# Optimization experiments

Measured on AMD Instinct MI355X. Metric: run time of the kernel, lower is better.

Reference implementation:

```python
import jax, jax.numpy as jnp
import numpy as np

B, S, D = 4, 1024, 1024
H, DH = 16, 64
F = 4 * D
EPS = 1e-6


def _ln(x, scale, bias, axes=-1):
    mean = jnp.mean(x, axis=axes, keepdims=True)
    var = jnp.var(x, axis=axes, keepdims=True)
    return (x - mean) * jax.lax.rsqrt(var + EPS) * scale + bias


def setup_inputs() -> dict:
    key = jax.random.key(0)
    ks = jax.random.split(key, 20)
    sd = 1.0 / np.sqrt(D)
    sf = 1.0 / np.sqrt(F)
    inp = {
        'x': jax.random.normal(ks[0], (B, S, D), jnp.float32),
        'z': jax.random.normal(ks[1], (B, S, D), jnp.float32),
        'ln1_s': jnp.ones((D,), jnp.float32),
        'ln1_b': jnp.zeros((D,), jnp.float32),
        'Wq': jax.random.normal(ks[2], (D, D), jnp.float32) * sd,
        'bq': jnp.zeros((D,), jnp.float32),
        'Wk': jax.random.normal(ks[3], (D, D), jnp.float32) * sd,
        'bk': jnp.zeros((D,), jnp.float32),
        'Wv': jax.random.normal(ks[4], (D, D), jnp.float32) * sd,
        'bv': jnp.zeros((D,), jnp.float32),
        'qn_s': jnp.ones((H, DH), jnp.float32),
        'qn_b': jnp.zeros((H, DH), jnp.float32),
        'kn_s': jnp.ones((H, DH), jnp.float32),
        'kn_b': jnp.zeros((H, DH), jnp.float32),
        'Wo': jax.random.normal(ks[5], (D, D), jnp.float32) * sd,
        'bo': jnp.zeros((D,), jnp.float32),
        'ln2_s': jnp.ones((D,), jnp.float32),
        'ln2_b': jnp.zeros((D,), jnp.float32),
        'W1': jax.random.normal(ks[6], (D, F), jnp.float32) * sd,
        'b1': jnp.zeros((F,), jnp.float32),
        'W2': jax.random.normal(ks[7], (D, F), jnp.float32) * sd,
        'b2': jnp.zeros((F,), jnp.float32),
        'W3': jax.random.normal(ks[8], (F, D), jnp.float32) * sf,
        'b3': jnp.zeros((D,), jnp.float32),
    }
    return inp


def reference(x, z, ln1_s, ln1_b, Wq, bq, Wk, bk, Wv, bv, qn_s, qn_b, kn_s, kn_b,
              Wo, bo, ln2_s, ln2_b, W1, b1, W2, b2, W3, b3):
    # z is unused by the original module body
    x_skip = x
    xn = _ln(x, ln1_s, ln1_b)
    q = (xn @ Wq + bq).reshape(B, S, H, DH)
    k = (xn @ Wk + bk).reshape(B, S, H, DH)
    v = (xn @ Wv + bv).reshape(B, S, H, DH)
    # QK-norm: flax LayerNorm(feature_axes=(-2,-1)) still reduces over axis -1,
    # but carries (H, DH)-shaped scale/bias
    q = _ln(q, qn_s, qn_b)
    k = _ln(k, kn_s, kn_b)
    attn = jnp.einsum('bqhd,bkhd->bhqk', q, k) / jnp.sqrt(jnp.asarray(DH, q.dtype))
    attn = jax.nn.softmax(attn, axis=-1)
    out = jnp.einsum('bhqk,bkhd->bqhd', attn, v).reshape(B, S, D)
    x = x_skip + out @ Wo + bo
    x_skip = x
    xn = _ln(x, ln2_s, ln2_b)
    x1 = xn @ W1 + b1
    x2 = xn @ W2 + b2
    h = x1 * jax.nn.gelu(x2, approximate=True)  # GeGLU
    x = x_skip + h @ W3 + b3
    return x
```

## Files before the change

kernel.cpp:

```cpp
#include <hip/hip_runtime.h>

typedef unsigned short u16;
typedef __bf16  bfrag  __attribute__((ext_vector_type(8)));
typedef float   f32x4  __attribute__((ext_vector_type(4)));
typedef u16     u16x8  __attribute__((ext_vector_type(8)));
typedef u16     u16x4  __attribute__((ext_vector_type(4)));

__device__ __forceinline__ float bf2f(u16 u) {
    unsigned v = ((unsigned)u) << 16;
    return __builtin_bit_cast(float, v);
}
__device__ __forceinline__ u16 f2bf(float f) {
    unsigned x = __builtin_bit_cast(unsigned, f);
    unsigned r = (x + 0x7fffu + ((x >> 16) & 1u)) >> 16;
    return (u16)r;
}
__device__ __forceinline__ void g2l16(const u16* g, u16* l) {
    __builtin_amdgcn_global_load_lds((__attribute__((address_space(1))) void*)g,
                                     (__attribute__((address_space(3))) void*)l, 16, 0, 0);
}
__device__ __forceinline__ float gelu_tanh(float x) {
    float c = 1.5957691216057308f * (x + 0.044715f * x * x * x);
    return x * __frcp_rn(1.0f + __expf(-c));
}

#define SWZ(lane)  ((((lane) & 3) ^ (((lane) >> 3) & 3)) * 8)
#define RSWZ(quad, l15)  ((((quad) ^ (((l15) >> 1) & 3))) * 8)

__global__ __launch_bounds__(256) void wt_all(
        const float* __restrict__ Wq, const float* __restrict__ Wk,
        const float* __restrict__ Wv, const float* __restrict__ Wo,
        const float* __restrict__ W1, const float* __restrict__ W2,
        const float* __restrict__ W3,
        u16* __restrict__ WqkvT, u16* __restrict__ WoT,
        u16* __restrict__ W12T, u16* __restrict__ W3T) {
    int blk = blockIdx.x;
    const float* W; u16* Wt; int R, C, local;
    if (blk < 3072) {
        int w = blk >> 10; local = blk & 1023;
        W = (w == 0) ? Wq : (w == 1) ? Wk : Wv;
        Wt = WqkvT + (size_t)w * 1024 * 1024; R = 1024; C = 1024;
    } else if (blk < 4096) { W = Wo; Wt = WoT; R = 1024; C = 1024; local = blk - 3072; }
    else if (blk < 8192)   { W = W1; Wt = W12T; R = 1024; C = 4096; local = blk - 4096; }
    else if (blk < 12288)  { W = W2; Wt = W12T + (size_t)4096 * 1024; R = 1024; C = 4096; local = blk - 8192; }
    else                   { W = W3; Wt = W3T; R = 4096; C = 1024; local = blk - 12288; }
    int tiles_x = C >> 5;
    int c0 = (local % tiles_x) * 32, r0 = (local / tiles_x) * 32;

    __shared__ float tile[32][33];
    int tx = threadIdx.x & 31, ty = threadIdx.x >> 5;
#pragma unroll
    for (int i = 0; i < 32; i += 8)
        tile[ty + i][tx] = W[(size_t)(r0 + ty + i) * C + c0 + tx];
    __syncthreads();
#pragma unroll
    for (int i = 0; i < 32; i += 8)
        Wt[(size_t)(c0 + ty + i) * R + r0 + tx] = f2bf(tile[tx][ty + i]);
}

__global__ __launch_bounds__(256) void ln1024(const float* __restrict__ x,
                                              const float* __restrict__ s,
                                              const float* __restrict__ bi,
                                              u16* __restrict__ out) {
    int row = blockIdx.x, t = threadIdx.x;
    const float4* xr = (const float4*)(x + (size_t)row * 1024);
    float4 v = xr[t];
    float sum = v.x + v.y + v.z + v.w;
    float sq  = v.x * v.x + v.y * v.y + v.z * v.z + v.w * v.w;
#pragma unroll
    for (int off = 1; off < 64; off <<= 1) {
        sum += __shfl_xor(sum, off);
        sq  += __shfl_xor(sq,  off);
    }
    __shared__ float s1[4], s2[4];
    int wave = t >> 6;
    if ((t & 63) == 0) { s1[wave] = sum; s2[wave] = sq; }
    __syncthreads();
    sum = s1[0] + s1[1] + s1[2] + s1[3];
    sq  = s2[0] + s2[1] + s2[2] + s2[3];
    float mean = sum * (1.0f / 1024.0f);
    float var  = sq  * (1.0f / 1024.0f) - mean * mean;
    float inv  = rsqrtf(var + 1e-6f);
    float4 sc = ((const float4*)s)[t], bb = ((const float4*)bi)[t];
    u16x4 o;
    o[0] = f2bf((v.x - mean) * inv * sc.x + bb.x);
    o[1] = f2bf((v.y - mean) * inv * sc.y + bb.y);
    o[2] = f2bf((v.z - mean) * inv * sc.z + bb.z);
    o[3] = f2bf((v.w - mean) * inv * sc.w + bb.w);
    *(u16x4*)&out[(size_t)row * 1024 + t * 4] = o;
}

#define BM 128
#define BK 32
template <int EPI, int BN_, int BSEL>
__global__ __launch_bounds__(256) void gemm_bt(const u16* __restrict__ A,
                                               const u16* __restrict__ Bt,
                                               const float* __restrict__ bias,
                                               const float* __restrict__ bias2,
                                               const float* __restrict__ bias3,
                                               const float* __restrict__ res,
                                               const float* __restrict__ qn_s,
                                               const float* __restrict__ qn_b,
                                               const float* __restrict__ kn_s,
                                               const float* __restrict__ kn_b,
                                               void* __restrict__ Cout,
                                               int M, int N, int K) {
    __shared__ u16 As[BM * BK];
    __shared__ u16 Bs[BN_ * BK];
    constexpr int MI = (BN_ == 128) ? 4 : 2;
    constexpr int NI = 4;
    int tid = threadIdx.x, wave = tid >> 6, lane = tid & 63;
    int quad = lane >> 4, l15 = lane & 15;
    int row0 = blockIdx.y * BM, col0 = blockIdx.x * BN_;
    int wr = (BN_ == 128) ? (wave >> 1) * 64 : wave * 32;
    int wc = (BN_ == 128) ? (wave & 1) * 64 : 0;
    int swz = SWZ(lane);
    int rswz = RSWZ(quad, l15);

    f32x4 acc[MI][NI] = {};

    const u16* gA = A + (size_t)(row0 + wave * 32 + (lane >> 2)) * K + swz;
    u16* lA = &As[wave * 32 * BK];
    const u16* gB;
    u16* lB;
    if (BN_ == 128) { gB = Bt + (size_t)(col0 + wave * 32 + (lane >> 2)) * K + swz; lB = &Bs[wave * 32 * BK]; }
    else            { gB = Bt + (size_t)(col0 + wave * 16 + (lane >> 2)) * K + swz; lB = &Bs[wave * 16 * BK]; }

    for (int k0 = 0; k0 < K; k0 += BK) {
        __syncthreads();
        g2l16(gA + k0,          lA);
        g2l16(gA + k0 + 16 * K, lA + 16 * BK);
        if (BN_ == 128) {
            g2l16(gB + k0,          lB);
            g2l16(gB + k0 + 16 * K, lB + 16 * BK);
        } else {
            g2l16(gB + k0, lB);
        }
        __syncthreads();
        bfrag af[MI], bf[NI];
#pragma unroll
        for (int mi = 0; mi < MI; mi++)
            af[mi] = *(const bfrag*)&As[(wr + mi * 16 + l15) * BK + rswz];
#pragma unroll
        for (int ni = 0; ni < NI; ni++)
            bf[ni] = *(const bfrag*)&Bs[(wc + ni * 16 + l15) * BK + rswz];
#pragma unroll
        for (int mi = 0; mi < MI; mi++)
#pragma unroll
            for (int ni = 0; ni < NI; ni++)
                acc[mi][ni] = __builtin_amdgcn_mfma_f32_16x16x32_bf16(
                    af[mi], bf[ni], acc[mi][ni], 0, 0, 0);
    }

    float bv[NI];
    int cols[NI];
#pragma unroll
    for (int ni = 0; ni < NI; ni++) {
        cols[ni] = col0 + wc + ni * 16 + l15;
        if (BSEL == 1) {
            int seg = cols[ni] >> 10;
            const float* bp = (seg == 0) ? bias : (seg == 1) ? bias2 : bias3;
            bv[ni] = bp[cols[ni] & 1023];
        } else {
            bv[ni] = bias[cols[ni]];
        }
    }

    if (EPI == 4) {
        int cbase = col0 + wc;
        int z = cbase >> 10;
        int hd = (cbase >> 6) & 15;
        float post = (z == 0) ? 0.125f : 1.0f;
        float sn[NI], bn[NI];
        if (z < 2) {
            const float* ns = (z == 0) ? qn_s : kn_s;
            const float* nb = (z == 0) ? qn_b : kn_b;
#pragma unroll
            for (int ni = 0; ni < NI; ni++) {
                sn[ni] = ns[hd * 64 + ni * 16 + l15];
                bn[ni] = nb[hd * 64 + ni * 16 + l15];
            }
        }
#pragma unroll
        for (int mi = 0; mi < MI; mi++) {
            int rbase = row0 + wr + mi * 16 + quad * 4;
#pragma unroll
            for (int r = 0; r < 4; r++) {
                float v0 = acc[mi][0][r] + bv[0];
                float v1 = acc[mi][1][r] + bv[1];
                float v2 = acc[mi][2][r] + bv[2];
                float v3 = acc[mi][3][r] + bv[3];
                size_t rb = (size_t)(rbase + r) * N + cbase;
                if (z == 2) {
                    ((u16*)Cout)[rb + 0 * 16 + l15] = f2bf(v0);
                    ((u16*)Cout)[rb + 1 * 16 + l15] = f2bf(v1);
                    ((u16*)Cout)[rb + 2 * 16 + l15] = f2bf(v2);
                    ((u16*)Cout)[rb + 3 * 16 + l15] = f2bf(v3);
                } else {
                    float s  = v0 + v1 + v2 + v3;
                    float sq = v0 * v0 + v1 * v1 + v2 * v2 + v3 * v3;
#pragma unroll
                    for (int m = 1; m < 16; m <<= 1) {
                        s  += __shfl_xor(s,  m);
                        sq += __shfl_xor(sq, m);
                    }
                    float mean = s * (1.0f / 64.0f);
                    float var  = sq * (1.0f / 64.0f) - mean * mean;
                    float inv  = rsqrtf(var + 1e-6f);
                    ((u16*)Cout)[rb + 0 * 16 + l15] = f2bf(((v0 - mean) * inv * sn[0] + bn[0]) * post);
                    ((u16*)Cout)[rb + 1 * 16 + l15] = f2bf(((v1 - mean) * inv * sn[1] + bn[1]) * post);
                    ((u16*)Cout)[rb + 2 * 16 + l15] = f2bf(((v2 - mean) * inv * sn[2] + bn[2]) * post);
                    ((u16*)Cout)[rb + 3 * 16 + l15] = f2bf(((v3 - mean) * inv * sn[3] + bn[3]) * post);
                }
            }
        }
        return;
    }

#pragma unroll
    for (int mi = 0; mi < MI; mi++) {
        int rbase = row0 + wr + mi * 16 + quad * 4;
#pragma unroll
        for (int r = 0; r < 4; r++) {
            int row = rbase + r;
#pragma unroll
            for (int ni = 0; ni < NI; ni++) {
                float val = acc[mi][ni][r] + bv[ni];
                size_t idx = (size_t)row * N + cols[ni];
                if (EPI == 1) {
                    ((u16*)Cout)[idx] = f2bf(val);
                } else {
                    ((float*)Cout)[idx] = val + res[idx];
                }
            }
        }
    }
}

__global__ __launch_bounds__(256, 2) void gemm_w12(const u16* __restrict__ A,
                                                   const u16* __restrict__ W12T,
                                                   const float* __restrict__ b1,
                                                   const float* __restrict__ b2,
                                                   u16* __restrict__ H) {
    __shared__ u16 As[128 * BK];
    __shared__ u16 B1s[128 * BK];
    __shared__ u16 B2s[128 * BK];
    int tid = threadIdx.x, wave = tid >> 6, lane = tid & 63;
    int quad = lane >> 4, l15 = lane & 15;
    int row0 = blockIdx.y * 128, col0 = blockIdx.x * 128;
    int wr = (wave >> 1) * 64, wc = (wave & 1) * 64;
    int swz = SWZ(lane);
    int rswz = RSWZ(quad, l15);

    f32x4 acc1[4][4] = {}, acc2[4][4] = {};

    const u16* gA  = A    + (size_t)(row0 + wave * 32 + (lane >> 2)) * 1024 + swz;
    const u16* gB1 = W12T + (size_t)(col0 + wave * 32 + (lane >> 2)) * 1024 + swz;
    const u16* gB2 = gB1  + (size_t)4096 * 1024;
    u16* lA  = &As [wave * 32 * BK];
    u16* lB1 = &B1s[wave * 32 * BK];
    u16* lB2 = &B2s[wave * 32 * BK];

    for (int k0 = 0; k0 < 1024; k0 += BK) {
        __syncthreads();
        g2l16(gA  + k0,             lA);
        g2l16(gA  + k0 + 16 * 1024, lA  + 16 * BK);
        g2l16(gB1 + k0,             lB1);
        g2l16(gB1 + k0 + 16 * 1024, lB1 + 16 * BK);
        g2l16(gB2 + k0,             lB2);
        g2l16(gB2 + k0 + 16 * 1024, lB2 + 16 * BK);
        __syncthreads();
        bfrag af[4], b1f[4], b2f[4];
#pragma unroll
        for (int mi = 0; mi < 4; mi++)
            af[mi] = *(const bfrag*)&As[(wr + mi * 16 + l15) * BK + rswz];
#pragma unroll
        for (int ni = 0; ni < 4; ni++) {
            b1f[ni] = *(const bfrag*)&B1s[(wc + ni * 16 + l15) * BK + rswz];
            b2f[ni] = *(const bfrag*)&B2s[(wc + ni * 16 + l15) * BK + rswz];
        }
#pragma unroll
        for (int mi = 0; mi < 4; mi++)
#pragma unroll
            for (int ni = 0; ni < 4; ni++) {
                acc1[mi][ni] = __builtin_amdgcn_mfma_f32_16x16x32_bf16(
                    af[mi], b1f[ni], acc1[mi][ni], 0, 0, 0);
                acc2[mi][ni] = __builtin_amdgcn_mfma_f32_16x16x32_bf16(
                    af[mi], b2f[ni], acc2[mi][ni], 0, 0, 0);
            }
    }

    float bv1[4], bv2[4];
    int cols[4];
#pragma unroll
    for (int ni = 0; ni < 4; ni++) {
        cols[ni] = col0 + wc + ni * 16 + l15;
        bv1[ni] = b1[cols[ni]];
        bv2[ni] = b2[cols[ni]];
    }
#pragma unroll
    for (int mi = 0; mi < 4; mi++) {
        int rbase = row0 + wr + mi * 16 + quad * 4;
#pragma unroll
        for (int r = 0; r < 4; r++) {
#pragma unroll
            for (int ni = 0; ni < 4; ni++) {
                float x1 = acc1[mi][ni][r] + bv1[ni];
                float x2 = acc2[mi][ni][r] + bv2[ni];
                H[(size_t)(rbase + r) * 4096 + cols[ni]] = f2bf(x1 * gelu_tanh(x2));
            }
        }
    }
}

__global__ __launch_bounds__(256) void gemm_splitk(const u16* __restrict__ A,
                                                   const u16* __restrict__ Bt,
                                                   u16* __restrict__ p0,
                                                   u16* __restrict__ p1,
                                                   u16* __restrict__ p2,
                                                   u16* __restrict__ p3) {
    const int K = 4096, N = 1024;
    __shared__ u16 As[128 * BK];
    __shared__ u16 Bs[128 * BK];
    int tid = threadIdx.x, wave = tid >> 6, lane = tid & 63;
    int quad = lane >> 4, l15 = lane & 15;
    int row0 = blockIdx.y * 128, col0 = blockIdx.x * 128;
    int kz = blockIdx.z;
    u16* P = (kz == 0) ? p0 : (kz == 1) ? p1 : (kz == 2) ? p2 : p3;
    int wr = (wave >> 1) * 64, wc = (wave & 1) * 64;
    int swz = SWZ(lane);
    int rswz = RSWZ(quad, l15);

    f32x4 acc[4][4] = {};

    const u16* gA = A  + (size_t)(row0 + wave * 32 + (lane >> 2)) * K + kz * 1024 + swz;
    const u16* gB = Bt + (size_t)(col0 + wave * 32 + (lane >> 2)) * K + kz * 1024 + swz;
    u16* lA = &As[wave * 32 * BK];
    u16* lB = &Bs[wave * 32 * BK];

    for (int k0 = 0; k0 < 1024; k0 += BK) {
        __syncthreads();
        g2l16(gA + k0,          lA);
        g2l16(gA + k0 + 16 * K, lA + 16 * BK);
        g2l16(gB + k0,          lB);
        g2l16(gB + k0 + 16 * K, lB + 16 * BK);
        __syncthreads();
        bfrag af[4], bf[4];
#pragma unroll
        for (int mi = 0; mi < 4; mi++)
            af[mi] = *(const bfrag*)&As[(wr + mi * 16 + l15) * BK + rswz];
#pragma unroll
        for (int ni = 0; ni < 4; ni++)
            bf[ni] = *(const bfrag*)&Bs[(wc + ni * 16 + l15) * BK + rswz];
#pragma unroll
        for (int mi = 0; mi < 4; mi++)
#pragma unroll
            for (int ni = 0; ni < 4; ni++)
                acc[mi][ni] = __builtin_amdgcn_mfma_f32_16x16x32_bf16(
                    af[mi], bf[ni], acc[mi][ni], 0, 0, 0);
    }

#pragma unroll
    for (int mi = 0; mi < 4; mi++) {
        int rbase = row0 + wr + mi * 16 + quad * 4;
#pragma unroll
        for (int r = 0; r < 4; r++)
#pragma unroll
            for (int ni = 0; ni < 4; ni++)
                P[(size_t)(rbase + r) * N + wc + col0 + ni * 16 + l15] =
                    f2bf(acc[mi][ni][r]);
    }
}

__global__ __launch_bounds__(256) void reduce4(const u16* __restrict__ p0,
                                               const u16* __restrict__ p1,
                                               const u16* __restrict__ p2,
                                               const u16* __restrict__ p3,
                                               const float* __restrict__ xmid,
                                               const float* __restrict__ b3,
                                               float* __restrict__ out) {
    size_t i = ((size_t)blockIdx.x * 256 + threadIdx.x) * 4;
    float4 xm = *(const float4*)&xmid[i];
    float4 bb = *(const float4*)&b3[i & 1023];
    u16x4 a0 = *(const u16x4*)&p0[i];
    u16x4 a1 = *(const u16x4*)&p1[i];
    u16x4 a2 = *(const u16x4*)&p2[i];
    u16x4 a3 = *(const u16x4*)&p3[i];
    float4 o;
    o.x = xm.x + bb.x + bf2f(a0[0]) + bf2f(a1[0]) + bf2f(a2[0]) + bf2f(a3[0]);
    o.y = xm.y + bb.y + bf2f(a0[1]) + bf2f(a1[1]) + bf2f(a2[1]) + bf2f(a3[1]);
    o.z = xm.z + bb.z + bf2f(a0[2]) + bf2f(a1[2]) + bf2f(a2[2]) + bf2f(a3[2]);
    o.w = xm.w + bb.w + bf2f(a0[3]) + bf2f(a1[3]) + bf2f(a2[3]) + bf2f(a3[3]);
    *(float4*)&out[i] = o;
}

#define LP 72
__global__ __launch_bounds__(256) void flash(const u16* __restrict__ qkv,
                                             u16* __restrict__ o) {
    int qt = blockIdx.x, h = blockIdx.y, b = blockIdx.z;
    int tid = threadIdx.x, wave = tid >> 6, lane = tid & 63;
    int quad = lane >> 4, l15 = lane & 15;

    __shared__ u16 Qs[128 * LP];
    __shared__ u16 Ks[64 * LP];
    __shared__ u16 Vt[64 * LP];
    __shared__ u16 Ps[128 * LP];

    {
        int row = tid >> 1, half = tid & 1;
        const u16* src = qkv + (size_t)(b * 1024 + qt * 128 + row) * 3072 + h * 64 + half * 32;
        u16* dst = &Qs[row * LP + half * 32];
#pragma unroll
        for (int i = 0; i < 4; i++)
            ((u16x8*)dst)[i] = ((const u16x8*)src)[i];
    }

    f32x4 accO[2][4] = {};
    float m_run[2][4], l_run[2][4];
#pragma unroll
    for (int rt = 0; rt < 2; rt++)
#pragma unroll
        for (int r = 0; r < 4; r++) { m_run[rt][r] = -1e30f; l_run[rt][r] = 0.0f; }

    for (int kt = 0; kt < 16; kt++) {
        __syncthreads();
        {
            int row = tid >> 2, seg = tid & 3;
            size_t gb = (size_t)(b * 1024 + kt * 64 + row) * 3072 + h * 64;
            const u16* ksrc = qkv + gb + 1024 + seg * 16;
            *(u16x8*)&Ks[row * LP + seg * 16]     = *(const u16x8*)ksrc;
            *(u16x8*)&Ks[row * LP + seg * 16 + 8] = *(const u16x8*)(ksrc + 8);
            const u16* vsrc = qkv + gb + 2048 + seg * 16;
            u16x8 v0 = *(const u16x8*)vsrc, v1 = *(const u16x8*)(vsrc + 8);
#pragma unroll
            for (int j = 0; j < 8; j++) Vt[(seg * 16 + j) * LP + row]     = v0[j];
#pragma unroll
            for (int j = 0; j < 8; j++) Vt[(seg * 16 + 8 + j) * LP + row] = v1[j];
        }
        __syncthreads();

        f32x4 accS[2][4] = {};
#pragma unroll
        for (int kk = 0; kk < 2; kk++) {
            bfrag aq[2];
#pragma unroll
            for (int rt = 0; rt < 2; rt++)
                aq[rt] = *(const bfrag*)&Qs[(wave * 32 + rt * 16 + l15) * LP + kk * 32 + quad * 8];
#pragma unroll
            for (int ct = 0; ct < 4; ct++) {
                bfrag bk = *(const bfrag*)&Ks[(ct * 16 + l15) * LP + kk * 32 + quad * 8];
                accS[0][ct] = __builtin_amdgcn_mfma_f32_16x16x32_bf16(aq[0], bk, accS[0][ct], 0, 0, 0);
                accS[1][ct] = __builtin_amdgcn_mfma_f32_16x16x32_bf16(aq[1], bk, accS[1][ct], 0, 0, 0);
            }
        }

#pragma unroll
        for (int rt = 0; rt < 2; rt++) {
#pragma unroll
            for (int r = 0; r < 4; r++) {
                float tmax = accS[rt][0][r];
#pragma unroll
                for (int ct = 1; ct < 4; ct++) tmax = fmaxf(tmax, accS[rt][ct][r]);
#pragma unroll
                for (int m = 1; m < 16; m <<= 1) tmax = fmaxf(tmax, __shfl_xor(tmax, m));
                float mnew  = fmaxf(m_run[rt][r], tmax);
                float alpha = __expf(m_run[rt][r] - mnew);
                float lsum = 0.0f;
                float p[4];
#pragma unroll
                for (int ct = 0; ct < 4; ct++) {
                    p[ct] = __expf(accS[rt][ct][r] - mnew);
                    lsum += p[ct];
                }
#pragma unroll
                for (int m = 1; m < 16; m <<= 1) lsum += __shfl_xor(lsum, m);
                l_run[rt][r] = l_run[rt][r] * alpha + lsum;
                m_run[rt][r] = mnew;
#pragma unroll
                for (int oc = 0; oc < 4; oc++) accO[rt][oc][r] *= alpha;
                int prow = wave * 32 + rt * 16 + quad * 4 + r;
#pragma unroll
                for (int ct = 0; ct < 4; ct++)
                    Ps[prow * LP + ct * 16 + l15] = f2bf(p[ct]);
            }
        }

#pragma unroll
        for (int kk = 0; kk < 2; kk++) {
            bfrag ap[2];
#pragma unroll
            for (int rt = 0; rt < 2; rt++)
                ap[rt] = *(const bfrag*)&Ps[(wave * 32 + rt * 16 + l15) * LP + kk * 32 + quad * 8];
#pragma unroll
            for (int oc = 0; oc < 4; oc++) {
                bfrag bv = *(const bfrag*)&Vt[(oc * 16 + l15) * LP + kk * 32 + quad * 8];
                accO[0][oc] = __builtin_amdgcn_mfma_f32_16x16x32_bf16(ap[0], bv, accO[0][oc], 0, 0, 0);
                accO[1][oc] = __builtin_amdgcn_mfma_f32_16x16x32_bf16(ap[1], bv, accO[1][oc], 0, 0, 0);
            }
        }
    }

#pragma unroll
    for (int rt = 0; rt < 2; rt++) {
#pragma unroll
        for (int r = 0; r < 4; r++) {
            int srow = qt * 128 + wave * 32 + rt * 16 + quad * 4 + r;
            float linv = 1.0f / l_run[rt][r];
#pragma unroll
            for (int oc = 0; oc < 4; oc++)
                o[(size_t)(b * 1024 + srow) * 1024 + h * 64 + oc * 16 + l15] =
                    f2bf(accO[rt][oc][r] * linv);
        }
    }
}

extern "C" void kernel_launch(void* const* d_in, const int* in_sizes, int n_in,
                              void* d_out, int out_size, void* d_ws, size_t ws_size,
                              hipStream_t stream) {
    const float* x     = (const float*)d_in[0];
    const float* ln1_s = (const float*)d_in[2];
    const float* ln1_b = (const float*)d_in[3];
    const float* Wq = (const float*)d_in[4];  const float* bq = (const float*)d_in[5];
    const float* Wk = (const float*)d_in[6];  const float* bk = (const float*)d_in[7];
    const float* Wv = (const float*)d_in[8];  const float* bv = (const float*)d_in[9];
    const float* qn_s = (const float*)d_in[10]; const float* qn_b = (const float*)d_in[11];
    const float* kn_s = (const float*)d_in[12]; const float* kn_b = (const float*)d_in[13];
    const float* Wo = (const float*)d_in[14]; const float* bo = (const float*)d_in[15];
    const float* ln2_s = (const float*)d_in[16]; const float* ln2_b = (const float*)d_in[17];
    const float* W1 = (const float*)d_in[18]; const float* b1 = (const float*)d_in[19];
    const float* W2 = (const float*)d_in[20]; const float* b2 = (const float*)d_in[21];
    const float* W3 = (const float*)d_in[22]; const float* b3 = (const float*)d_in[23];
    float* out = (float*)d_out;

    char* ws = (char*)d_ws;
    const size_t MB = (size_t)1 << 20;
    u16* WqkvT = (u16*)(ws + 0);
    u16* WoT   = (u16*)(ws + 6 * MB);
    u16* W12T  = (u16*)(ws + 8 * MB);
    u16* W3T   = (u16*)(ws + 24 * MB);
    u16* xn1   = (u16*)(ws + 32 * MB);
    u16* attn  = (u16*)(ws + 32 * MB);
    u16* xn2   = (u16*)(ws + 32 * MB);
    u16* qkv   = (u16*)(ws + 40 * MB);
    float* xmid = (float*)(ws + 40 * MB);
    u16* p3    = (u16*)(ws + 56 * MB);
    u16* h     = (u16*)(ws + 64 * MB);
    u16* p0    = (u16*)(ws + 0);
    u16* p1    = (u16*)(ws + 8 * MB);
    u16* p2    = (u16*)(ws + 16 * MB);

    dim3 blk(256);

    wt_all<<<16384, blk, 0, stream>>>(Wq, Wk, Wv, Wo, W1, W2, W3,
                                      WqkvT, WoT, W12T, W3T);

    ln1024<<<4096, blk, 0, stream>>>(x, ln1_s, ln1_b, xn1);

    gemm_bt<4, 128, 1><<<dim3(24, 32), blk, 0, stream>>>(
        xn1, WqkvT, bq, bk, bv, nullptr, qn_s, qn_b, kn_s, kn_b,
        qkv, 4096, 3072, 1024);

    flash<<<dim3(8, 16, 4), blk, 0, stream>>>(qkv, attn);

    gemm_bt<2, 64, 0><<<dim3(16, 32), blk, 0, stream>>>(
        attn, WoT, bo, nullptr, nullptr, x, nullptr, nullptr, nullptr, nullptr,
        xmid, 4096, 1024, 1024);

    ln1024<<<4096, blk, 0, stream>>>(xmid, ln2_s, ln2_b, xn2);

    gemm_w12<<<dim3(32, 32), blk, 0, stream>>>(xn2, W12T, b1, b2, h);

    gemm_splitk<<<dim3(8, 32, 4), blk, 0, stream>>>(h, W3T, p0, p1, p2, p3);

    reduce4<<<4096, blk, 0, stream>>>(p0, p1, p2, p3, xmid, b3, out);
}
```

Measured before the change: 452.2 us.

## Use 2-wave 128x128 GEMM tiles for QKV and split-K, fuse LN1 into transpose

Measured after the change: 515.3 us. +14.0%, slower.

```diff
diff --git a/kernel.cpp b/kernel.cpp
--- a/kernel.cpp
+++ b/kernel.cpp
@@ -26,15 +26,48 @@
 
 #define SWZ(lane)  ((((lane) & 3) ^ (((lane) >> 3) & 3)) * 8)
 #define RSWZ(quad, l15)  ((((quad) ^ (((l15) >> 1) & 3))) * 8)
-
-__global__ __launch_bounds__(256) void wt_all(
+#define BK 32
+
+__global__ __launch_bounds__(256) void wtln(
         const float* __restrict__ Wq, const float* __restrict__ Wk,
         const float* __restrict__ Wv, const float* __restrict__ Wo,
         const float* __restrict__ W1, const float* __restrict__ W2,
         const float* __restrict__ W3,
         u16* __restrict__ WqkvT, u16* __restrict__ WoT,
-        u16* __restrict__ W12T, u16* __restrict__ W3T) {
+        u16* __restrict__ W12T, u16* __restrict__ W3T,
+        const float* __restrict__ x, const float* __restrict__ ln1_s,
+        const float* __restrict__ ln1_b, u16* __restrict__ xn1) {
+    __shared__ float tile[32][33];
     int blk = blockIdx.x;
+    if (blk >= 16384) {
+        int row = blk - 16384, t = threadIdx.x;
+        float4 v = ((const float4*)(x + (size_t)row * 1024))[t];
+        float sum = v.x + v.y + v.z + v.w;
+        float sq  = v.x * v.x + v.y * v.y + v.z * v.z + v.w * v.w;
+#pragma unroll
+        for (int off = 1; off < 64; off <<= 1) {
+            sum += __shfl_xor(sum, off);
+            sq  += __shfl_xor(sq,  off);
+        }
+        float* s1 = &tile[0][0];
+        float* s2 = &tile[0][8];
+        int wave = t >> 6;
+        if ((t & 63) == 0) { s1[wave] = sum; s2[wave] = sq; }
+        __syncthreads();
+        sum = s1[0] + s1[1] + s1[2] + s1[3];
+        sq  = s2[0] + s2[1] + s2[2] + s2[3];
+        float mean = sum * (1.0f / 1024.0f);
+        float var  = sq  * (1.0f / 1024.0f) - mean * mean;
+        float inv  = rsqrtf(var + 1e-6f);
+        float4 sc = ((const float4*)ln1_s)[t], bb = ((const float4*)ln1_b)[t];
+        u16x4 o;
+        o[0] = f2bf((v.x - mean) * inv * sc.x + bb.x);
+        o[1] = f2bf((v.y - mean) * inv * sc.y + bb.y);
+        o[2] = f2bf((v.z - mean) * inv * sc.z + bb.z);
+        o[3] = f2bf((v.w - mean) * inv * sc.w + bb.w);
+        *(u16x4*)&xn1[(size_t)row * 1024 + t * 4] = o;
+        return;
+    }
     const float* W; u16* Wt; int R, C, local;
     if (blk < 3072) {
         int w = blk >> 10; local = blk & 1023;
@@ -46,8 +79,6 @@
     else                   { W = W3; Wt = W3T; R = 4096; C = 1024; local = blk - 12288; }
     int tiles_x = C >> 5;
     int c0 = (local % tiles_x) * 32, r0 = (local / tiles_x) * 32;
-
-    __shared__ float tile[32][33];
     int tx = threadIdx.x & 31, ty = threadIdx.x >> 5;
 #pragma unroll
     for (int i = 0; i < 32; i += 8)
@@ -63,8 +94,7 @@
                                               const float* __restrict__ bi,
                                               u16* __restrict__ out) {
     int row = blockIdx.x, t = threadIdx.x;
-    const float4* xr = (const float4*)(x + (size_t)row * 1024);
-    float4 v = xr[t];
+    float4 v = ((const float4*)(x + (size_t)row * 1024))[t];
     float sum = v.x + v.y + v.z + v.w;
     float sq  = v.x * v.x + v.y * v.y + v.z * v.z + v.w * v.w;
 #pragma unroll
@@ -90,28 +120,142 @@
     *(u16x4*)&out[(size_t)row * 1024 + t * 4] = o;
 }
 
-#define BM 128
-#define BK 32
-template <int EPI, int BN_, int BSEL>
+template <int EPI>
+__global__ __launch_bounds__(128) void gemm2(const u16* __restrict__ A,
+                                             const u16* __restrict__ Bt,
+                                             const float* __restrict__ bias,
+                                             const float* __restrict__ bias2,
+                                             const float* __restrict__ bias3,
+                                             const float* __restrict__ qn_s,
+                                             const float* __restrict__ qn_b,
+                                             const float* __restrict__ kn_s,
+                                             const float* __restrict__ kn_b,
+                                             u16* __restrict__ p0,
+                                             u16* __restrict__ p1,
+                                             u16* __restrict__ p2,
+                                             u16* __restrict__ p3,
+                                             int M, int N, int K, int Klen) {
+    __shared__ u16 As[128 * BK];
+    __shared__ u16 Bs[128 * BK];
+    int tid = threadIdx.x, wave = tid >> 6, lane = tid & 63;
+    int quad = lane >> 4, l15 = lane & 15;
+    int row0 = blockIdx.y * 128, col0 = blockIdx.x * 128;
+    int kz = blockIdx.z;
+    int swz = SWZ(lane);
+    int rswz = RSWZ(quad, l15);
+
+    f32x4 acc[8][4] = {};
+
+    const u16* gA = A  + (size_t)(row0 + wave * 64 + (lane >> 2)) * K + kz * Klen + swz;
+    const u16* gB = Bt + (size_t)(col0 + wave * 64 + (lane >> 2)) * K + kz * Klen + swz;
+    u16* lA = &As[wave * 64 * BK];
+    u16* lB = &Bs[wave * 64 * BK];
+
+    for (int k0 = 0; k0 < Klen; k0 += BK) {
+        __syncthreads();
+#pragma unroll
+        for (int j = 0; j < 4; j++) {
+            g2l16(gA + k0 + j * 16 * K, lA + j * 16 * BK);
+            g2l16(gB + k0 + j * 16 * K, lB + j * 16 * BK);
+        }
+        __syncthreads();
+        bfrag af[8], bf[4];
+#pragma unroll
+        for (int mi = 0; mi < 8; mi++)
+            af[mi] = *(const bfrag*)&As[(mi * 16 + l15) * BK + rswz];
+#pragma unroll
+        for (int ni = 0; ni < 4; ni++)
+            bf[ni] = *(const bfrag*)&Bs[(wave * 64 + ni * 16 + l15) * BK + rswz];
+#pragma unroll
+        for (int mi = 0; mi < 8; mi++)
+#pragma unroll
+            for (int ni = 0; ni < 4; ni++)
+                acc[mi][ni] = __builtin_amdgcn_mfma_f32_16x16x32_bf16(
+                    af[mi], bf[ni], acc[mi][ni], 0, 0, 0);
+    }
+
+    if (EPI == 0) {
+        u16* P = (kz == 0) ? p0 : (kz == 1) ? p1 : (kz == 2) ? p2 : p3;
+#pragma unroll
+        for (int mi = 0; mi < 8; mi++) {
+            int rbase = row0 + mi * 16 + quad * 4;
+#pragma unroll
+            for (int r = 0; r < 4; r++)
+#pragma unroll
+                for (int ni = 0; ni < 4; ni++)
+                    P[(size_t)(rbase + r) * N + col0 + wave * 64 + ni * 16 + l15] =
+                        f2bf(acc[mi][ni][r]);
+        }
+    } else {
+        int cbase = col0 + wave * 64;
+        int z = cbase >> 10;
+        int hd = (cbase >> 6) & 15;
+        const float* bp = (z == 0) ? bias : (z == 1) ? bias2 : bias3;
+        float post = (z == 0) ? 0.125f : 1.0f;
+        float bv[4], sn[4], bn[4];
+#pragma unroll
+        for (int ni = 0; ni < 4; ni++)
+            bv[ni] = bp[(cbase & 1023) + ni * 16 + l15];
+        if (z < 2) {
+            const float* ns = (z == 0) ? qn_s : kn_s;
+            const float* nb = (z == 0) ? qn_b : kn_b;
+#pragma unroll
+            for (int ni = 0; ni < 4; ni++) {
+                sn[ni] = ns[hd * 64 + ni * 16 + l15];
+                bn[ni] = nb[hd * 64 + ni * 16 + l15];
+            }
+        }
+        u16* Cout = p0;
+#pragma unroll
+        for (int mi = 0; mi < 8; mi++) {
+            int rbase = row0 + mi * 16 + quad * 4;
+#pragma unroll
+            for (int r = 0; r < 4; r++) {
+                float v0 = acc[mi][0][r] + bv[0];
+                float v1 = acc[mi][1][r] + bv[1];
+                float v2 = acc[mi][2][r] + bv[2];
+                float v3 = acc[mi][3][r] + bv[3];
+                size_t rb = (size_t)(rbase + r) * N + cbase;
+                if (z == 2) {
+                    Cout[rb + 0 * 16 + l15] = f2bf(v0);
+                    Cout[rb + 1 * 16 + l15] = f2bf(v1);
+                    Cout[rb + 2 * 16 + l15] = f2bf(v2);
+                    Cout[rb + 3 * 16 + l15] = f2bf(v3);
+                } else {
+                    float s  = v0 + v1 + v2 + v3;
+                    float sq = v0 * v0 + v1 * v1 + v2 * v2 + v3 * v3;
+#pragma unroll
+                    for (int m = 1; m < 16; m <<= 1) {
+                        s  += __shfl_xor(s,  m);
+                        sq += __shfl_xor(sq, m);
+                    }
+                    float mean = s * (1.0f / 64.0f);
+                    float var  = sq * (1.0f / 64.0f) - mean * mean;
+                    float inv  = rsqrtf(var + 1e-6f);
+                    Cout[rb + 0 * 16 + l15] = f2bf(((v0 - mean) * inv * sn[0] + bn[0]) * post);
+                    Cout[rb + 1 * 16 + l15] = f2bf(((v1 - mean) * inv * sn[1] + bn[1]) * post);
+                    Cout[rb + 2 * 16 + l15] = f2bf(((v2 - mean) * inv * sn[2] + bn[2]) * post);
+                    Cout[rb + 3 * 16 + l15] = f2bf(((v3 - mean) * inv * sn[3] + bn[3]) * post);
+                }
+            }
+        }
+    }
+}
+
+template <int EPI, int BN_>
 __global__ __launch_bounds__(256) void gemm_bt(const u16* __restrict__ A,
                                                const u16* __restrict__ Bt,
                                                const float* __restrict__ bias,
-                                               const float* __restrict__ bias2,
-                                               const float* __restrict__ bias3,
                                                const float* __restrict__ res,
-                                               const float* __restrict__ qn_s,
-                                               const float* __restrict__ qn_b,
-                                               const float* __restrict__ kn_s,
-                                               const float* __restrict__ kn_b,
                                                void* __restrict__ Cout,
                                                int M, int N, int K) {
-    __shared__ u16 As[BM * BK];
+    __shared__ u16 As[128 * BK];
     __shared__ u16 Bs[BN_ * BK];
     constexpr int MI = (BN_ == 128) ? 4 : 2;
     constexpr int NI = 4;
     int tid = threadIdx.x, wave = tid >> 6, lane = tid & 63;
     int quad = lane >> 4, l15 = lane & 15;
-    int row0 = blockIdx.y * BM, col0 = blockIdx.x * BN_;
+    int row0 = blockIdx.y * 128, col0 = blockIdx.x * BN_;
     int wr = (BN_ == 128) ? (wave >> 1) * 64 : wave * 32;
     int wc = (BN_ == 128) ? (wave & 1) * 64 : 0;
     int swz = SWZ(lane);
@@ -157,66 +301,8 @@
 #pragma unroll
     for (int ni = 0; ni < NI; ni++) {
         cols[ni] = col0 + wc + ni * 16 + l15;
-        if (BSEL == 1) {
-            int seg = cols[ni] >> 10;
-            const float* bp = (seg == 0) ? bias : (seg == 1) ? bias2 : bias3;
-            bv[ni] = bp[cols[ni] & 1023];
-        } else {
-            bv[ni] = bias[cols[ni]];
-        }
-    }
-
-    if (EPI == 4) {
-        int cbase = col0 + wc;
-        int z = cbase >> 10;
-        int hd = (cbase >> 6) & 15;
-        float post = (z == 0) ? 0.125f : 1.0f;
-        float sn[NI], bn[NI];
-        if (z < 2) {
-            const float* ns = (z == 0) ? qn_s : kn_s;
-            const float* nb = (z == 0) ? qn_b : kn_b;
-#pragma unroll
-            for (int ni = 0; ni < NI; ni++) {
-                sn[ni] = ns[hd * 64 + ni * 16 + l15];
-                bn[ni] = nb[hd * 64 + ni * 16 + l15];
-            }
-        }
-#pragma unroll
-        for (int mi = 0; mi < MI; mi++) {
-            int rbase = row0 + wr + mi * 16 + quad * 4;
-#pragma unroll
-            for (int r = 0; r < 4; r++) {
-                float v0 = acc[mi][0][r] + bv[0];
-                float v1 = acc[mi][1][r] + bv[1];
-                float v2 = acc[mi][2][r] + bv[2];
-                float v3 = acc[mi][3][r] + bv[3];
-                size_t rb = (size_t)(rbase + r) * N + cbase;
-                if (z == 2) {
-                    ((u16*)Cout)[rb + 0 * 16 + l15] = f2bf(v0);
-                    ((u16*)Cout)[rb + 1 * 16 + l15] = f2bf(v1);
-                    ((u16*)Cout)[rb + 2 * 16 + l15] = f2bf(v2);
-                    ((u16*)Cout)[rb + 3 * 16 + l15] = f2bf(v3);
-                } else {
-                    float s  = v0 + v1 + v2 + v3;
-                    float sq = v0 * v0 + v1 * v1 + v2 * v2 + v3 * v3;
-#pragma unroll
-                    for (int m = 1; m < 16; m <<= 1) {
-                        s  += __shfl_xor(s,  m);
-                        sq += __shfl_xor(sq, m);
-                    }
-                    float mean = s * (1.0f / 64.0f);
-                    float var  = sq * (1.0f / 64.0f) - mean * mean;
-                    float inv  = rsqrtf(var + 1e-6f);
-                    ((u16*)Cout)[rb + 0 * 16 + l15] = f2bf(((v0 - mean) * inv * sn[0] + bn[0]) * post);
-                    ((u16*)Cout)[rb + 1 * 16 + l15] = f2bf(((v1 - mean) * inv * sn[1] + bn[1]) * post);
-                    ((u16*)Cout)[rb + 2 * 16 + l15] = f2bf(((v2 - mean) * inv * sn[2] + bn[2]) * post);
-                    ((u16*)Cout)[rb + 3 * 16 + l15] = f2bf(((v3 - mean) * inv * sn[3] + bn[3]) * post);
-                }
-            }
-        }
-        return;
-    }
-
+        bv[ni]   = bias[cols[ni]];
+    }
 #pragma unroll
     for (int mi = 0; mi < MI; mi++) {
         int rbase = row0 + wr + mi * 16 + quad * 4;
@@ -227,11 +313,7 @@
             for (int ni = 0; ni < NI; ni++) {
                 float val = acc[mi][ni][r] + bv[ni];
                 size_t idx = (size_t)row * N + cols[ni];
-                if (EPI == 1) {
-                    ((u16*)Cout)[idx] = f2bf(val);
-                } else {
-                    ((float*)Cout)[idx] = val + res[idx];
-                }
+                ((float*)Cout)[idx] = val + res[idx];
             }
         }
     }
@@ -310,65 +392,6 @@
                 H[(size_t)(rbase + r) * 4096 + cols[ni]] = f2bf(x1 * gelu_tanh(x2));
             }
         }
-    }
-}
-
-__global__ __launch_bounds__(256) void gemm_splitk(const u16* __restrict__ A,
-                                                   const u16* __restrict__ Bt,
-                                                   u16* __restrict__ p0,
-                                                   u16* __restrict__ p1,
-                                                   u16* __restrict__ p2,
-                                                   u16* __restrict__ p3) {
-    const int K = 4096, N = 1024;
-    __shared__ u16 As[128 * BK];
-    __shared__ u16 Bs[128 * BK];
-    int tid = threadIdx.x, wave = tid >> 6, lane = tid & 63;
-    int quad = lane >> 4, l15 = lane & 15;
-    int row0 = blockIdx.y * 128, col0 = blockIdx.x * 128;
-    int kz = blockIdx.z;
-    u16* P = (kz == 0) ? p0 : (kz == 1) ? p1 : (kz == 2) ? p2 : p3;
-    int wr = (wave >> 1) * 64, wc = (wave & 1) * 64;
-    int swz = SWZ(lane);
-    int rswz = RSWZ(quad, l15);
-
-    f32x4 acc[4][4] = {};
-
-    const u16* gA = A  + (size_t)(row0 + wave * 32 + (lane >> 2)) * K + kz * 1024 + swz;
-    const u16* gB = Bt + (size_t)(col0 + wave * 32 + (lane >> 2)) * K + kz * 1024 + swz;
-    u16* lA = &As[wave * 32 * BK];
-    u16* lB = &Bs[wave * 32 * BK];
-
-    for (int k0 = 0; k0 < 1024; k0 += BK) {
-        __syncthreads();
-        g2l16(gA + k0,          lA);
-        g2l16(gA + k0 + 16 * K, lA + 16 * BK);
-        g2l16(gB + k0,          lB);
-        g2l16(gB + k0 + 16 * K, lB + 16 * BK);
-        __syncthreads();
-        bfrag af[4], bf[4];
-#pragma unroll
-        for (int mi = 0; mi < 4; mi++)
-            af[mi] = *(const bfrag*)&As[(wr + mi * 16 + l15) * BK + rswz];
-#pragma unroll
-        for (int ni = 0; ni < 4; ni++)
-            bf[ni] = *(const bfrag*)&Bs[(wc + ni * 16 + l15) * BK + rswz];
-#pragma unroll
-        for (int mi = 0; mi < 4; mi++)
-#pragma unroll
-            for (int ni = 0; ni < 4; ni++)
-                acc[mi][ni] = __builtin_amdgcn_mfma_f32_16x16x32_bf16(
-                    af[mi], bf[ni], acc[mi][ni], 0, 0, 0);
-    }
-
-#pragma unroll
-    for (int mi = 0; mi < 4; mi++) {
-        int rbase = row0 + wr + mi * 16 + quad * 4;
-#pragma unroll
-        for (int r = 0; r < 4; r++)
-#pragma unroll
-            for (int ni = 0; ni < 4; ni++)
-                P[(size_t)(rbase + r) * N + wc + col0 + ni * 16 + l15] =
-                    f2bf(acc[mi][ni][r]);
     }
 }
 
@@ -549,28 +572,26 @@
     u16* p1    = (u16*)(ws + 8 * MB);
     u16* p2    = (u16*)(ws + 16 * MB);
 
-    dim3 blk(256);
-
-    wt_all<<<16384, blk, 0, stream>>>(Wq, Wk, Wv, Wo, W1, W2, W3,
-                                      WqkvT, WoT, W12T, W3T);
-
-    ln1024<<<4096, blk, 0, stream>>>(x, ln1_s, ln1_b, xn1);
-
-    gemm_bt<4, 128, 1><<<dim3(24, 32), blk, 0, stream>>>(
-        xn1, WqkvT, bq, bk, bv, nullptr, qn_s, qn_b, kn_s, kn_b,
-        qkv, 4096, 3072, 1024);
-
-    flash<<<dim3(8, 16, 4), blk, 0, stream>>>(qkv, attn);
-
-    gemm_bt<2, 64, 0><<<dim3(16, 32), blk, 0, stream>>>(
-        attn, WoT, bo, nullptr, nullptr, x, nullptr, nullptr, nullptr, nullptr,
-        xmid, 4096, 1024, 1024);
-
-    ln1024<<<4096, blk, 0, stream>>>(xmid, ln2_s, ln2_b, xn2);
-
-    gemm_w12<<<dim3(32, 32), blk, 0, stream>>>(xn2, W12T, b1, b2, h);
-
-    gemm_splitk<<<dim3(8, 32, 4), blk, 0, stream>>>(h, W3T, p0, p1, p2, p3);
-
-    reduce4<<<4096, blk, 0, stream>>>(p0, p1, p2, p3, xmid, b3, out);
-}
+    wtln<<<20480, 256, 0, stream>>>(Wq, Wk, Wv, Wo, W1, W2, W3,
+                                    WqkvT, WoT, W12T, W3T,
+                                    x, ln1_s, ln1_b, xn1);
+
+    gemm2<4><<<dim3(24, 32), 128, 0, stream>>>(
+        xn1, WqkvT, bq, bk, bv, qn_s, qn_b, kn_s, kn_b,
+        qkv, nullptr, nullptr, nullptr, 4096, 3072, 1024, 1024);
+
+    flash<<<dim3(8, 16, 4), 256, 0, stream>>>(qkv, attn);
+
+    gemm_bt<2, 64><<<dim3(16, 32), 256, 0, stream>>>(
+        attn, WoT, bo, x, xmid, 4096, 1024, 1024);
+
+    ln1024<<<4096, 256, 0, stream>>>(xmid, ln2_s, ln2_b, xn2);
+
+    gemm_w12<<<dim3(32, 32), 256, 0, stream>>>(xn2, W12T, b1, b2, h);
+
+    gemm2<0><<<dim3(8, 32, 4), 128, 0, stream>>>(
+        h, W3T, nullptr, nullptr, nullptr, nullptr, nullptr, nullptr, nullptr,
+        p0, p1, p2, p3, 4096, 1024, 4096, 1024);
+
+    reduce4<<<4096, 256, 0, stream>>>(p0, p1, p2, p3, xmid, b3, out);
+}
```
